# Kernel tuning notes

Measured on AMD Instinct MI355X. Metric: run time of the kernel, lower is better.

## Reference

```python
import jax, jax.numpy as jnp
import numpy as np

D_MODEL = 1024
N_HEADS = 16
D_K = D_MODEL // N_HEADS  # 64
D_FF = 2688
THETA = 10000.0
EPS = 1e-5
B, S = 2, 2048


def _rmsnorm(x, w):
    xf = x.astype(jnp.float32)
    ms = jnp.mean(xf * xf, axis=-1, keepdims=True)
    return (xf * w * jax.lax.rsqrt(ms + EPS)).astype(x.dtype)


def _rope(x, cos, sin):
    # x: [B, S, H, D_K]; cos/sin: [S, D_K//2]
    xe = x[..., 0::2]
    xo = x[..., 1::2]
    c = cos[None, :, None, :]
    s = sin[None, :, None, :]
    re = xe * c - xo * s
    ro = xe * s + xo * c
    # interleave back to even/odd layout
    return jnp.stack([re, ro], axis=-1).reshape(x.shape)


def setup_inputs() -> dict:
    key = jax.random.key(0)
    ks = jax.random.split(key, 12)
    sc = 0.02  # keep activations numerically sane (stand-in for trunc_normal init)
    return {
        "x": jax.random.normal(ks[0], (B, S, D_MODEL), dtype=jnp.float32),
        "ln1_w": jax.random.normal(ks[1], (D_MODEL,), dtype=jnp.float32) * sc + 1.0,
        "q_w": jax.random.normal(ks[2], (D_MODEL, D_MODEL), dtype=jnp.float32) * sc,
        "k_w": jax.random.normal(ks[3], (D_MODEL, D_MODEL), dtype=jnp.float32) * sc,
        "v_w": jax.random.normal(ks[4], (D_MODEL, D_MODEL), dtype=jnp.float32) * sc,
        "o_w": jax.random.normal(ks[5], (D_MODEL, D_MODEL), dtype=jnp.float32) * sc,
        "ln2_w": jax.random.normal(ks[6], (D_MODEL,), dtype=jnp.float32) * sc + 1.0,
        "w1_w": jax.random.normal(ks[7], (D_FF, D_MODEL), dtype=jnp.float32) * sc,
        "w3_w": jax.random.normal(ks[8], (D_FF, D_MODEL), dtype=jnp.float32) * sc,
        "w2_w": jax.random.normal(ks[9], (D_MODEL, D_FF), dtype=jnp.float32) * sc,
        "token_positions": jnp.arange(S, dtype=jnp.int32),
    }


def reference(x, ln1_w, q_w, k_w, v_w, o_w, ln2_w, w1_w, w3_w, w2_w, token_positions):
    b, s, _ = x.shape
    # --- pre-norm attention sublayer ---
    h = _rmsnorm(x, ln1_w)
    Q = (h @ q_w.T).reshape(b, s, N_HEADS, D_K)
    K = (h @ k_w.T).reshape(b, s, N_HEADS, D_K)
    V = (h @ v_w.T).reshape(b, s, N_HEADS, D_K)

    # RoPE tables from token positions
    pos = token_positions.astype(jnp.float32)                      # [S]
    kk = jnp.arange(D_K // 2, dtype=jnp.float32)
    inv_freq = THETA ** (-2.0 * kk / D_K)                          # [D_K/2]
    ang = pos[:, None] * inv_freq[None, :]                          # [S, D_K/2]
    cos, sin = jnp.cos(ang), jnp.sin(ang)

    Qr = _rope(Q, cos, sin)
    Kr = _rope(K, cos, sin)

    scale = 1.0 / jnp.sqrt(jnp.float32(D_K))
    scores = jnp.einsum("bqhd,bkhd->bhqk", Qr, Kr) * scale          # [B,H,S,S]
    causal = jnp.tril(jnp.ones((s, s), dtype=bool))
    scores = jnp.where(causal[None, None], scores, jnp.float32(-10000.0))
    attn = jax.nn.softmax(scores, axis=-1)
    ctx = jnp.einsum("bhqk,bkhd->bqhd", attn, V).reshape(b, s, D_MODEL)
    x1 = x + ctx @ o_w.T

    # --- pre-norm SwiGLU FFN sublayer ---
    h2 = _rmsnorm(x1, ln2_w)
    g = h2 @ w1_w.T                                                 # [B,S,D_FF]
    u = h2 @ w3_w.T
    ffn = (g * jax.nn.sigmoid(g) * u) @ w2_w.T
    return x1 + ffn
```

## Files before the change

kernel.cpp:

```cpp
#include <hip/hip_runtime.h>
#include <cstdint>

#define DM   1024
#define NH   16
#define DK   64
#define DFF  2688
#define SEQ  2048
#define BB   2
#define MTOT (BB*SEQ)

typedef __attribute__((ext_vector_type(8))) short short8;
typedef __attribute__((ext_vector_type(4))) float f32x4;

typedef const __attribute__((address_space(1))) void* gaddr_t;
typedef __attribute__((address_space(3))) void* laddr_t;
#define GLOAD_LDS16(g, l) __builtin_amdgcn_global_load_lds((gaddr_t)(g), (laddr_t)(l), 16, 0, 0)
#define MFMA16(a, b, c) __builtin_amdgcn_mfma_f32_16x16x32_bf16((a), (b), (c), 0, 0, 0)
#define WAIT_LDS() __builtin_amdgcn_s_waitcnt(0xc07f)

#define VMCNT(n) asm volatile("s_waitcnt vmcnt(" #n ")" ::: "memory")
#define BAR() do { asm volatile("" ::: "memory"); \
                   __builtin_amdgcn_s_barrier();  \
                   asm volatile("" ::: "memory"); } while (0)

__device__ __forceinline__ float bf2f(unsigned short u) {
    union { unsigned int i; float f; } v; v.i = ((unsigned int)u) << 16; return v.f;
}
__device__ __forceinline__ unsigned short f2bf(float f) {
    union { float f; unsigned int i; } v; v.f = f;
    unsigned int r = v.i + 0x7fffu + ((v.i >> 16) & 1u);
    return (unsigned short)(r >> 16);
}
__device__ __forceinline__ unsigned long long pack4bf(float a, float b, float c, float d) {
    return (unsigned long long)f2bf(a) | ((unsigned long long)f2bf(b) << 16)
         | ((unsigned long long)f2bf(c) << 32) | ((unsigned long long)f2bf(d) << 48);
}

__device__ __forceinline__ void band_swizzle(int& bx, int& by) {
    const int gx = gridDim.x;
    const int lin = blockIdx.y * gx + blockIdx.x;
    const int xcd = lin & 7, k = lin >> 3;
    by = xcd * 4 + (k & 3);
    bx = k >> 2;
}

__global__ __launch_bounds__(256)
void prep_k(const float* __restrict__ q_w, const float* __restrict__ k_w,
            const float* __restrict__ v_w, const float* __restrict__ o_w,
            const float* __restrict__ w1_w, const float* __restrict__ w3_w,
            const float* __restrict__ w2_w,
            unsigned short* __restrict__ Wqkv, unsigned short* __restrict__ Wo,
            unsigned short* __restrict__ W13, unsigned short* __restrict__ W2) {
    const int blk = blockIdx.x;
    const float* src; unsigned short* dst; int cols, rmul, roff, i;
    if (blk < 4096) {
        const int rr = blk >> 10;
        i = (blk & 1023) * 256 + threadIdx.x;
        cols = 1024; rmul = 1;
        if (rr == 0)      { src = q_w; dst = Wqkv; roff = 0; }
        else if (rr == 1) { src = k_w; dst = Wqkv; roff = 1024; }
        else if (rr == 2) { src = v_w; dst = Wqkv; roff = 2048; }
        else              { src = o_w; dst = Wo;   roff = 0; }
    } else if (blk < 6784) {
        i = (blk - 4096) * 256 + threadIdx.x; src = w1_w; dst = W13; cols = 1024; rmul = 2; roff = 0;
    } else if (blk < 9472) {
        i = (blk - 6784) * 256 + threadIdx.x; src = w3_w; dst = W13; cols = 1024; rmul = 2; roff = 1;
    } else {
        i = (blk - 9472) * 256 + threadIdx.x; src = w2_w; dst = W2;  cols = 2688; rmul = 1; roff = 0;
    }
    const int e = i * 4;
    const int r = e / cols, c = e - r * cols;
    const float4 v = *(const float4*)(src + e);
    ushort4 o;
    o.x = f2bf(v.x); o.y = f2bf(v.y); o.z = f2bf(v.z); o.w = f2bf(v.w);
    *(ushort4*)(dst + (size_t)(r * rmul + roff) * cols + c) = o;
}

__global__ __launch_bounds__(256)
void rmsnorm_k(const float* __restrict__ x, const float* __restrict__ w,
               unsigned short* __restrict__ out) {
    const int row = blockIdx.x;
    const int tid = threadIdx.x;
    const float4 v = ((const float4*)(x + (size_t)row * DM))[tid];
    float ss = v.x * v.x + v.y * v.y + v.z * v.z + v.w * v.w;
#pragma unroll
    for (int off = 32; off > 0; off >>= 1) ss += __shfl_down(ss, off, 64);
    __shared__ float sred[4];
    const int wave = tid >> 6, lane = tid & 63;
    if (lane == 0) sred[wave] = ss;
    __syncthreads();
    const float tot = sred[0] + sred[1] + sred[2] + sred[3];
    const float rinv = rsqrtf(tot * (1.0f / DM) + 1e-5f);
    const float4 wv = ((const float4*)w)[tid];
    ushort4 o;
    o.x = f2bf(v.x * wv.x * rinv);
    o.y = f2bf(v.y * wv.y * rinv);
    o.z = f2bf(v.z * wv.z * rinv);
    o.w = f2bf(v.w * wv.w * rinv);
    ((ushort4*)(out + (size_t)row * DM))[tid] = o;
}

__global__ __launch_bounds__(256)
void rope_tab_k(const int* __restrict__ pos, float* __restrict__ tab) {
    const int tid = threadIdx.x;
    const int s = blockIdx.x * 4 + (tid >> 6);
    const int t = tid & 63;
    const int kk = t & 31;
    const float ang = (float)pos[s] * __expf(-0.28782313662f * (float)kk);
    tab[s * 64 + t] = (t < 32) ? cosf(ang) : sinf(ang);
}

template <int EPI>
__global__ __launch_bounds__(512)
void gemm256(const unsigned short* __restrict__ A,
             const unsigned short* __restrict__ B,
             unsigned short* __restrict__ O0,
             unsigned short* __restrict__ O1,
             unsigned short* __restrict__ O2,
             const float* __restrict__ ROPT,
             int N, int K) {
    __shared__ unsigned short As[2][16384];
    __shared__ unsigned short Bs[2][12288];
    const int tid = threadIdx.x;
    const int wave = tid >> 6, lane = tid & 63;
    const int l15 = lane & 15, quad = lane >> 4;

    const int gx = gridDim.x;
    const int nwg = gx * gridDim.y;
    const int lin = blockIdx.y * gx + blockIdx.x;
    const int swz = (lin & 7) * (nwg >> 3) + (lin >> 3);
    const int bx = swz % gx, by = swz / gx;
    const int m0 = by * 256, n0 = bx * 192;
    const int wr = (wave >> 2) * 128, wc = (wave & 3) * 48;

    const f32x4 z4 = {0.f, 0.f, 0.f, 0.f};
    f32x4 acc[8][3];
#pragma unroll
    for (int m = 0; m < 8; m++)
#pragma unroll
        for (int n = 0; n < 3; n++) acc[m][n] = z4;

    const unsigned short* pa[4];
    int la[4];
#pragma unroll
    for (int r = 0; r < 4; r++) {
        const int s = r * 512 + tid;
        pa[r] = A + (size_t)(m0 + (s & 255)) * K + (s >> 8) * 8;
        la[r] = (r * 512 + wave * 64) * 8;
    }
    const unsigned short* pb[3];
    int lb[3];
#pragma unroll
    for (int r = 0; r < 3; r++) {
        const int s = r * 512 + tid;
        const int bk = s / 192, br = s - bk * 192;
        pb[r] = B + (size_t)(n0 + br) * K + bk * 8;
        lb[r] = (r * 512 + wave * 64) * 8;
    }

    const int nt = K >> 6;

#pragma unroll
    for (int r = 0; r < 4; r++) { GLOAD_LDS16(pa[r], &As[0][la[r]]); pa[r] += 64; }
#pragma unroll
    for (int r = 0; r < 3; r++) { GLOAD_LDS16(pb[r], &Bs[0][lb[r]]); pb[r] += 64; }

    int cur = 0;
    for (int t = 0; t < nt; ++t) {
        const int nb = cur ^ 1;
        if (t + 1 < nt) {
#pragma unroll
            for (int r = 0; r < 4; r++) { GLOAD_LDS16(pa[r], &As[nb][la[r]]); pa[r] += 64; }
            VMCNT(4);
        } else {
            VMCNT(0);
        }
        BAR();

        short8 bg[3][2];
#pragma unroll
        for (int n = 0; n < 3; n++)
#pragma unroll
            for (int kk = 0; kk < 2; kk++)
                bg[n][kk] = *(const short8*)(&Bs[cur][((quad + 4 * kk) * 192 + wc + n * 16 + l15) * 8]);

        short8 afA[2][2], afB[2][2];
#pragma unroll
        for (int m = 0; m < 2; m++)
#pragma unroll
            for (int kk = 0; kk < 2; kk++)
                afA[m][kk] = *(const short8*)(&As[cur][((quad + 4 * kk) * 256 + wr + m * 16 + l15) * 8]);

#pragma unroll
        for (int p = 0; p < 4; ++p) {
            short8 (&afC)[2][2] = (p & 1) ? afB : afA;
            short8 (&afN)[2][2] = (p & 1) ? afA : afB;
            if (p < 3) {
#pragma unroll
                for (int m = 0; m < 2; m++)
#pragma unroll
                    for (int kk = 0; kk < 2; kk++)
                        afN[m][kk] = *(const short8*)(&As[cur][((quad + 4 * kk) * 256 + wr + ((p + 1) * 2 + m) * 16 + l15) * 8]);
            }
            if (p == 1 && t + 1 < nt) {
#pragma unroll
                for (int r = 0; r < 3; r++) { GLOAD_LDS16(pb[r], &Bs[nb][lb[r]]); pb[r] += 64; }
            }
            __builtin_amdgcn_s_setprio(1);
#pragma unroll
            for (int m = 0; m < 2; m++)
#pragma unroll
                for (int n = 0; n < 3; n++)
#pragma unroll
                    for (int kk = 0; kk < 2; kk++)
                        acc[p * 2 + m][n] = MFMA16(bg[n][kk], afC[m][kk], acc[p * 2 + m][n]);
            __builtin_amdgcn_s_setprio(0);
            BAR();
        }
        cur = nb;
    }

#pragma unroll
    for (int m = 0; m < 8; m++) {
        const int r = m0 + wr + m * 16 + l15;
        if (EPI == 0) {
            const int b = r >> 11, s = r & (SEQ - 1);
            const float* rt = ROPT + s * 64;
#pragma unroll
            for (int n = 0; n < 3; n++) {
                const int cb = n0 + wc + n * 16;
                const int sec = cb >> 10;
                const int h = (cb & 1023) >> 6;
                const int cc0 = (cb & 63) + quad * 4;
                const f32x4 a = acc[m][n];
                if (sec < 2) {
                    const int p0 = cc0 >> 1;
                    const float cA = rt[p0],     sA = rt[32 + p0];
                    const float cB = rt[p0 + 1], sB = rt[32 + p0 + 1];
                    const float e0 = a[0] * cA - a[1] * sA;
                    const float o0 = a[0] * sA + a[1] * cA;
                    const float e1 = a[2] * cB - a[3] * sB;
                    const float o1 = a[2] * sB + a[3] * cB;
                    unsigned short* dst = (sec == 0) ? O0 : O1;
                    *(unsigned long long*)(dst + ((size_t)(b * NH + h) * SEQ + s) * DK + cc0) =
                        pack4bf(e0, o0, e1, o1);
                } else {
                    unsigned short* dst = O2 + ((size_t)(b * NH + h) * DK) * SEQ + s;
#pragma unroll
                    for (int tq = 0; tq < 4; tq++)
                        dst[(size_t)(cc0 + tq) * SEQ] = f2bf(a[tq]);
                }
            }
        } else {
#pragma unroll
            for (int n = 0; n < 3; n++) {
                const int cc = n0 + wc + n * 16 + quad * 4;
                const f32x4 a = acc[m][n];
                const float s1 = a[0] * a[1] / (1.f + __expf(-a[0]));
                const float s2 = a[2] * a[3] / (1.f + __expf(-a[2]));
                *(unsigned int*)(O0 + (size_t)r * (DFF) + (cc >> 1)) =
                    (unsigned int)f2bf(s1) | ((unsigned int)f2bf(s2) << 16);
            }
        }
    }
}

__global__ __launch_bounds__(256, 4)
void gemm_thin(const unsigned short* __restrict__ A,
               const unsigned short* __restrict__ B,
               float* __restrict__ Cf,
               const float* __restrict__ R,
               int N, int K) {
    __shared__ unsigned short As[8192];
    __shared__ unsigned short Bs[4096];
    const int tid = threadIdx.x;
    const int wave = tid >> 6, lane = tid & 63;
    const int l15 = lane & 15, quad = lane >> 4;
    int bx, by;
    band_swizzle(bx, by);
    const int m0 = by * 128, n0 = bx * 64;
    const int wr = (wave & 1) * 64, wc = (wave >> 1) * 32;

    const f32x4 z4 = {0.f, 0.f, 0.f, 0.f};
    f32x4 acc[4][2];
#pragma unroll
    for (int i = 0; i < 4; i++)
#pragma unroll
        for (int j = 0; j < 2; j++) acc[i][j] = z4;

    const unsigned short* ap[4];
    int al[4];
#pragma unroll
    for (int i = 0; i < 4; i++) {
        const int s = i * 256 + tid;
        ap[i] = A + (size_t)(m0 + (s & 127)) * K + (s >> 7) * 8;
        al[i] = (i * 256 + wave * 64) * 8;
    }
    const unsigned short* bp[2];
    int bl[2];
#pragma unroll
    for (int i = 0; i < 2; i++) {
        const int s = i * 256 + tid;
        bp[i] = B + (size_t)(n0 + (s & 63)) * K + (s >> 6) * 8;
        bl[i] = (i * 256 + wave * 64) * 8;
    }

    const int nk = K >> 6;
    for (int kc = 0; kc < nk; kc++) {
        __syncthreads();
#pragma unroll
        for (int i = 0; i < 4; i++) { GLOAD_LDS16(ap[i], &As[al[i]]); ap[i] += 64; }
#pragma unroll
        for (int i = 0; i < 2; i++) { GLOAD_LDS16(bp[i], &Bs[bl[i]]); bp[i] += 64; }
        __syncthreads();
#pragma unroll
        for (int h = 0; h < 2; h++) {
            short8 af[4], bg[2];
#pragma unroll
            for (int t = 0; t < 4; t++)
                af[t] = *(const short8*)(&As[((quad + 4 * h) * 128 + wr + t * 16 + l15) * 8]);
#pragma unroll
            for (int t = 0; t < 2; t++)
                bg[t] = *(const short8*)(&Bs[((quad + 4 * h) * 64 + wc + t * 16 + l15) * 8]);
#pragma unroll
            for (int i = 0; i < 4; i++)
#pragma unroll
                for (int j = 0; j < 2; j++)
                    acc[i][j] = MFMA16(bg[j], af[i], acc[i][j]);
        }
    }

#pragma unroll
    for (int i = 0; i < 4; i++) {
        const int r = m0 + wr + i * 16 + l15;
#pragma unroll
        for (int j = 0; j < 2; j++) {
            const int cc = n0 + wc + j * 16 + quad * 4;
            const size_t idx = (size_t)r * N + cc;
            const float4 rv = *(const float4*)(R + idx);
            float4 ov;
            ov.x = acc[i][j][0] + rv.x;
            ov.y = acc[i][j][1] + rv.y;
            ov.z = acc[i][j][2] + rv.z;
            ov.w = acc[i][j][3] + rv.w;
            *(float4*)(Cf + idx) = ov;
        }
    }
}

template <bool MASK>
__device__ __forceinline__ void softmax_tile(f32x4 st[4], float& li, unsigned short* Pw,
                                             int l15, int quad, int j0, int myq) {
    float lsum = 0.f;
#pragma unroll
    for (int t = 0; t < 4; t++) {
#pragma unroll
        for (int r = 0; r < 4; r++) {
            float v = st[t][r] * 0.125f;
            if (MASK) {
                const int key = j0 + t * 16 + quad * 4 + r;
                if (key > myq) v = -1e30f;
            }
            const float p = __expf(v);
            st[t][r] = p;
            lsum += p;
        }
        *(unsigned long long*)(Pw + l15 * 72 + t * 16 + quad * 4) =
            pack4bf(st[t][0], st[t][1], st[t][2], st[t][3]);
    }
    li += lsum;
}

__global__ __launch_bounds__(256, 2)
void attn_k(const unsigned short* __restrict__ Qr, const unsigned short* __restrict__ Kr,
            const unsigned short* __restrict__ Vt, unsigned short* __restrict__ ctx) {
    __shared__ unsigned short KVl[2][8192];
    __shared__ unsigned short Pl[4 * 2 * 1152];
    const int tid = threadIdx.x;
    const int wave = tid >> 6, lane = tid & 63;
    const int l15 = lane & 15, quad = lane >> 4;
    const int bh = blockIdx.y, b = bh >> 4, h = bh & 15;
    const int g = blockIdx.x;
    const int qtA = g * 4 + wave, qtB = 127 - qtA;
    const int q0A = qtA * 16, q0B = qtB * 16;
    const int countA = g + 1, countB = 32 - g;
    const unsigned short* Kb = Kr + (size_t)bh * SEQ * DK;
    const unsigned short* Vb = Vt + (size_t)bh * DK * SEQ;

    const unsigned short* QbA = Qr + ((size_t)bh * SEQ + q0A) * DK;
    const unsigned short* QbB = Qr + ((size_t)bh * SEQ + q0B) * DK;
    const short8 qfA0 = *(const short8*)(QbA + l15 * DK + quad * 8);
    const short8 qfA1 = *(const short8*)(QbA + l15 * DK + 32 + quad * 8);
    const short8 qfB0 = *(const short8*)(QbB + l15 * DK + quad * 8);
    const short8 qfB1 = *(const short8*)(QbB + l15 * DK + 32 + quad * 8);

    const int slot0 = wave * 128 + lane, slot1 = slot0 + 64;
    const int ck0 = slot0 >> 3, s0 = slot0 & 7;
    const int ck1 = slot1 >> 3, s1 = slot1 & 7;
    const unsigned short* kp0 = Kb + ck0 * 64 + (s0 ^ (ck0 & 7)) * 8;
    const unsigned short* kp1 = Kb + ck1 * 64 + (s1 ^ (ck1 & 7)) * 8;
    const unsigned short* vp0 = Vb + ck0 * 2048 + (s0 ^ (ck0 & 7)) * 8;
    const unsigned short* vp1 = Vb + ck1 * 2048 + (s1 ^ (ck1 & 7)) * 8;
    const int kb0 = wave * 1024, kb1 = kb0 + 512;

    unsigned short* PA = Pl + (wave * 2 + 0) * 1152;
    unsigned short* PB = Pl + (wave * 2 + 1) * 1152;

    const f32x4 z4 = {0.f, 0.f, 0.f, 0.f};
    f32x4 oA[4], oB[4];
#pragma unroll
    for (int d = 0; d < 4; d++) { oA[d] = z4; oB[d] = z4; }
    float liA = 0.f, liB = 0.f;
    const int myqA = q0A + l15, myqB = q0B + l15;
    const int xr = l15 & 7;

    GLOAD_LDS16(kp0, &KVl[0][kb0]);
    GLOAD_LDS16(kp1, &KVl[0][kb1]);
    GLOAD_LDS16(vp0, &KVl[0][4096 + kb0]);
    GLOAD_LDS16(vp1, &KVl[0][4096 + kb1]);
    kp0 += 4096; kp1 += 4096; vp0 += 64; vp1 += 64;

    for (int j = 0; j < countB; ++j) {
        const int bf = j & 1;
        const unsigned short* Kl = KVl[bf];
        const unsigned short* Vl = KVl[bf] + 4096;
        __syncthreads();
        if (j + 1 < countB) {
            GLOAD_LDS16(kp0, &KVl[bf ^ 1][kb0]);
            GLOAD_LDS16(kp1, &KVl[bf ^ 1][kb1]);
            GLOAD_LDS16(vp0, &KVl[bf ^ 1][4096 + kb0]);
            GLOAD_LDS16(vp1, &KVl[bf ^ 1][4096 + kb1]);
            kp0 += 4096; kp1 += 4096; vp0 += 64; vp1 += 64;
        }
        const int j0 = j * 64;
        short8 kf[4][2];
#pragma unroll
        for (int t = 0; t < 4; t++) {
            const unsigned short* kr = Kl + (t * 16 + l15) * 64;
            kf[t][0] = *(const short8*)(kr + (quad ^ xr) * 8);
            kf[t][1] = *(const short8*)(kr + ((4 + quad) ^ xr) * 8);
        }
        f32x4 stB[4];
        __builtin_amdgcn_s_setprio(1);
#pragma unroll
        for (int t = 0; t < 4; t++)
            stB[t] = MFMA16(kf[t][1], qfB1, MFMA16(kf[t][0], qfB0, z4));
        __builtin_amdgcn_s_setprio(0);
        const bool doA = (j < countA);
        if (doA) {
            f32x4 stA[4];
            __builtin_amdgcn_s_setprio(1);
#pragma unroll
            for (int t = 0; t < 4; t++)
                stA[t] = MFMA16(kf[t][1], qfA1, MFMA16(kf[t][0], qfA0, z4));
            __builtin_amdgcn_s_setprio(0);
            if (j == countA - 1) softmax_tile<true >(stA, liA, PA, l15, quad, j0, myqA);
            else                 softmax_tile<false>(stA, liA, PA, l15, quad, j0, myqA);
        }
        if (j == countB - 1) softmax_tile<true >(stB, liB, PB, l15, quad, j0, myqB);
        else                 softmax_tile<false>(stB, liB, PB, l15, quad, j0, myqB);
        WAIT_LDS();
        short8 vf[4][2];
#pragma unroll
        for (int dt = 0; dt < 4; dt++) {
            const unsigned short* vr = Vl + (dt * 16 + l15) * 64;
            vf[dt][0] = *(const short8*)(vr + (quad ^ xr) * 8);
            vf[dt][1] = *(const short8*)(vr + ((4 + quad) ^ xr) * 8);
        }
        {
            const short8 pfB0 = *(const short8*)(PB + l15 * 72 + quad * 8);
            const short8 pfB1 = *(const short8*)(PB + l15 * 72 + 32 + quad * 8);
            __builtin_amdgcn_s_setprio(1);
#pragma unroll
            for (int dt = 0; dt < 4; dt++)
                oB[dt] = MFMA16(vf[dt][1], pfB1, MFMA16(vf[dt][0], pfB0, oB[dt]));
            __builtin_amdgcn_s_setprio(0);
        }
        if (doA) {
            const short8 pfA0 = *(const short8*)(PA + l15 * 72 + quad * 8);
            const short8 pfA1 = *(const short8*)(PA + l15 * 72 + 32 + quad * 8);
            __builtin_amdgcn_s_setprio(1);
#pragma unroll
            for (int dt = 0; dt < 4; dt++)
                oA[dt] = MFMA16(vf[dt][1], pfA1, MFMA16(vf[dt][0], pfA0, oA[dt]));
            __builtin_amdgcn_s_setprio(0);
        }
    }
    liA += __shfl_xor(liA, 16, 64); liA += __shfl_xor(liA, 32, 64);
    liB += __shfl_xor(liB, 16, 64); liB += __shfl_xor(liB, 32, 64);
    const float invA = 1.0f / liA, invB = 1.0f / liB;
#pragma unroll
    for (int dt = 0; dt < 4; dt++) {
        *(unsigned long long*)(PA + l15 * 72 + dt * 16 + quad * 4) =
            pack4bf(oA[dt][0] * invA, oA[dt][1] * invA, oA[dt][2] * invA, oA[dt][3] * invA);
        *(unsigned long long*)(PB + l15 * 72 + dt * 16 + quad * 4) =
            pack4bf(oB[dt][0] * invB, oB[dt][1] * invB, oB[dt][2] * invB, oB[dt][3] * invB);
    }
    WAIT_LDS();
    const int row = lane >> 2, seg = (lane & 3) * 8;
#pragma unroll
    for (int p = 0; p < 2; p++) {
        const int cs = seg + p * 32;
        const uint4 va = *(const uint4*)(PA + row * 72 + cs);
        *(uint4*)(ctx + ((size_t)b * SEQ + q0A + row) * DM + h * DK + cs) = va;
        const uint4 vb = *(const uint4*)(PB + row * 72 + cs);
        *(uint4*)(ctx + ((size_t)b * SEQ + q0B + row) * DM + h * DK + cs) = vb;
    }
}

extern "C" void kernel_launch(void* const* d_in, const int* in_sizes, int n_in,
                              void* d_out, int out_size, void* d_ws, size_t ws_size,
                              hipStream_t stream) {
    const float* x     = (const float*)d_in[0];
    const float* ln1_w = (const float*)d_in[1];
    const float* q_w   = (const float*)d_in[2];
    const float* k_w   = (const float*)d_in[3];
    const float* v_w   = (const float*)d_in[4];
    const float* o_w   = (const float*)d_in[5];
    const float* ln2_w = (const float*)d_in[6];
    const float* w1_w  = (const float*)d_in[7];
    const float* w3_w  = (const float*)d_in[8];
    const float* w2_w  = (const float*)d_in[9];
    const int*   tpos  = (const int*)d_in[10];
    float* out = (float*)d_out;
    char* ws = (char*)d_ws;

    unsigned short* Wqkv = (unsigned short*)(ws + 0);
    unsigned short* Wo   = (unsigned short*)(ws + 6291456);
    unsigned short* W13  = (unsigned short*)(ws + 8388608);
    unsigned short* W2   = (unsigned short*)(ws + 19398656);
    float*          X1   = (float*)(ws + 24903680);
    float*          ROPT = (float*)(ws + 24903680);
    char* base = ws + 41680896;
    unsigned short* H    = (unsigned short*)(base);
    unsigned short* QR   = (unsigned short*)(base + 8388608);
    unsigned short* KR   = (unsigned short*)(base + 16777216);
    unsigned short* VT   = (unsigned short*)(base + 25165824);
    unsigned short* CTX  = (unsigned short*)(base + 33554432);
    unsigned short* H2   = (unsigned short*)(base);
    unsigned short* ACT  = (unsigned short*)(base + 41943040);

    prep_k<<<12160, 256, 0, stream>>>(q_w, k_w, v_w, o_w, w1_w, w3_w, w2_w,
                                      Wqkv, Wo, W13, W2);
    rope_tab_k<<<512, 256, 0, stream>>>(tpos, ROPT);

    rmsnorm_k<<<4096, 256, 0, stream>>>(x, ln1_w, H);
    gemm256<0><<<dim3(16, 16), 512, 0, stream>>>(H, Wqkv, QR, KR, VT, ROPT, 3072, 1024);
    attn_k<<<dim3(16, 32), 256, 0, stream>>>(QR, KR, VT, CTX);
    gemm_thin<<<dim3(16, 32), 256, 0, stream>>>(CTX, Wo, X1, x, 1024, 1024);
    rmsnorm_k<<<4096, 256, 0, stream>>>(X1, ln2_w, H2);
    gemm256<1><<<dim3(28, 16), 512, 0, stream>>>(H2, W13, ACT, nullptr, nullptr, nullptr, 5376, 1024);
    gemm_thin<<<dim3(16, 32), 256, 0, stream>>>(ACT, W2, out, X1, 1024, 2688);
}
```

Measured before the change: 408.5 us.

## Double-buffer thin GEMM with 128x128 tiles, 512 threads and XCD swizzle

Rewrites the output-projection and down-projection GEMM to use 128x128 tiles with 8 waves. LDS is now double-buffered so the next K-slice loads overlap MFMA work, with vmcnt waits and s_setprio around the MFMA bursts. Block placement changes to a chunked XCD swizzle. Launching 256 blocks instead of 512 raises per-block reuse but lowers the number of workgroups and occupancy on a 256-CU device.

```diff
diff --git a/kernel.cpp b/kernel.cpp
--- a/kernel.cpp
+++ b/kernel.cpp
@@ -34,14 +34,6 @@
 __device__ __forceinline__ unsigned long long pack4bf(float a, float b, float c, float d) {
     return (unsigned long long)f2bf(a) | ((unsigned long long)f2bf(b) << 16)
          | ((unsigned long long)f2bf(c) << 32) | ((unsigned long long)f2bf(d) << 48);
-}
-
-__device__ __forceinline__ void band_swizzle(int& bx, int& by) {
-    const int gx = gridDim.x;
-    const int lin = blockIdx.y * gx + blockIdx.x;
-    const int xcd = lin & 7, k = lin >> 3;
-    by = xcd * 4 + (k & 3);
-    bx = k >> 2;
 }
 
 __global__ __launch_bounds__(256)
@@ -265,69 +257,95 @@
     }
 }
 
-__global__ __launch_bounds__(256, 4)
+__global__ __launch_bounds__(512)
 void gemm_thin(const unsigned short* __restrict__ A,
                const unsigned short* __restrict__ B,
                float* __restrict__ Cf,
                const float* __restrict__ R,
                int N, int K) {
-    __shared__ unsigned short As[8192];
-    __shared__ unsigned short Bs[4096];
+    __shared__ unsigned short As[2][8192];
+    __shared__ unsigned short Bs[2][8192];
     const int tid = threadIdx.x;
     const int wave = tid >> 6, lane = tid & 63;
     const int l15 = lane & 15, quad = lane >> 4;
-    int bx, by;
-    band_swizzle(bx, by);
-    const int m0 = by * 128, n0 = bx * 64;
-    const int wr = (wave & 1) * 64, wc = (wave >> 1) * 32;
+
+    const int gx = gridDim.x;
+    const int nwg = gx * gridDim.y;
+    const int lin = blockIdx.y * gx + blockIdx.x;
+    const int swz = (lin & 7) * (nwg >> 3) + (lin >> 3);
+    const int bx = swz % gx, by = swz / gx;
+    const int m0 = by * 128, n0 = bx * 128;
+    const int wr = (wave >> 2) * 64, wc = (wave & 3) * 32;
 
     const f32x4 z4 = {0.f, 0.f, 0.f, 0.f};
     f32x4 acc[4][2];
 #pragma unroll
-    for (int i = 0; i < 4; i++)
-#pragma unroll
-        for (int j = 0; j < 2; j++) acc[i][j] = z4;
-
-    const unsigned short* ap[4];
-    int al[4];
-#pragma unroll
-    for (int i = 0; i < 4; i++) {
-        const int s = i * 256 + tid;
-        ap[i] = A + (size_t)(m0 + (s & 127)) * K + (s >> 7) * 8;
-        al[i] = (i * 256 + wave * 64) * 8;
-    }
-    const unsigned short* bp[2];
-    int bl[2];
-#pragma unroll
-    for (int i = 0; i < 2; i++) {
-        const int s = i * 256 + tid;
-        bp[i] = B + (size_t)(n0 + (s & 63)) * K + (s >> 6) * 8;
-        bl[i] = (i * 256 + wave * 64) * 8;
-    }
-
-    const int nk = K >> 6;
-    for (int kc = 0; kc < nk; kc++) {
-        __syncthreads();
-#pragma unroll
-        for (int i = 0; i < 4; i++) { GLOAD_LDS16(ap[i], &As[al[i]]); ap[i] += 64; }
-#pragma unroll
-        for (int i = 0; i < 2; i++) { GLOAD_LDS16(bp[i], &Bs[bl[i]]); bp[i] += 64; }
-        __syncthreads();
-#pragma unroll
-        for (int h = 0; h < 2; h++) {
-            short8 af[4], bg[2];
-#pragma unroll
-            for (int t = 0; t < 4; t++)
-                af[t] = *(const short8*)(&As[((quad + 4 * h) * 128 + wr + t * 16 + l15) * 8]);
-#pragma unroll
-            for (int t = 0; t < 2; t++)
-                bg[t] = *(const short8*)(&Bs[((quad + 4 * h) * 64 + wc + t * 16 + l15) * 8]);
-#pragma unroll
-            for (int i = 0; i < 4; i++)
-#pragma unroll
-                for (int j = 0; j < 2; j++)
-                    acc[i][j] = MFMA16(bg[j], af[i], acc[i][j]);
-        }
+    for (int m = 0; m < 4; m++)
+#pragma unroll
+        for (int n = 0; n < 2; n++) acc[m][n] = z4;
+
+    const unsigned short* pa[2];
+    const unsigned short* pb[2];
+    int la[2], lb[2];
+#pragma unroll
+    for (int r = 0; r < 2; r++) {
+        const int s = r * 512 + tid;
+        pa[r] = A + (size_t)(m0 + (s & 127)) * K + (s >> 7) * 8;
+        pb[r] = B + (size_t)(n0 + (s & 127)) * K + (s >> 7) * 8;
+        la[r] = (r * 512 + wave * 64) * 8;
+        lb[r] = la[r];
+    }
+
+    const int nt = K >> 6;
+
+#pragma unroll
+    for (int r = 0; r < 2; r++) { GLOAD_LDS16(pa[r], &As[0][la[r]]); pa[r] += 64; }
+#pragma unroll
+    for (int r = 0; r < 2; r++) { GLOAD_LDS16(pb[r], &Bs[0][lb[r]]); pb[r] += 64; }
+
+    int cur = 0;
+    for (int t = 0; t < nt; ++t) {
+        const int nb = cur ^ 1;
+        if (t + 1 < nt) {
+#pragma unroll
+            for (int r = 0; r < 2; r++) { GLOAD_LDS16(pa[r], &As[nb][la[r]]); pa[r] += 64; }
+            VMCNT(2);
+        } else {
+            VMCNT(0);
+        }
+        BAR();
+
+        short8 bg[2][2];
+#pragma unroll
+        for (int n = 0; n < 2; n++)
+#pragma unroll
+            for (int kk = 0; kk < 2; kk++)
+                bg[n][kk] = *(const short8*)(&Bs[cur][((quad + 4 * kk) * 128 + wc + n * 16 + l15) * 8]);
+
+#pragma unroll
+        for (int p = 0; p < 2; ++p) {
+            if (p == 0 && t + 1 < nt) {
+#pragma unroll
+                for (int r = 0; r < 2; r++) { GLOAD_LDS16(pb[r], &Bs[nb][lb[r]]); pb[r] += 64; }
+            }
+            short8 af[2][2];
+#pragma unroll
+            for (int m = 0; m < 2; m++)
+#pragma unroll
+                for (int kk = 0; kk < 2; kk++)
+                    af[m][kk] = *(const short8*)(&As[cur][((quad + 4 * kk) * 128 + wr + (p * 2 + m) * 16 + l15) * 8]);
+            __builtin_amdgcn_s_setprio(1);
+#pragma unroll
+            for (int m = 0; m < 2; m++)
+#pragma unroll
+                for (int n = 0; n < 2; n++)
+#pragma unroll
+                    for (int kk = 0; kk < 2; kk++)
+                        acc[p * 2 + m][n] = MFMA16(bg[n][kk], af[m][kk], acc[p * 2 + m][n]);
+            __builtin_amdgcn_s_setprio(0);
+            BAR();
+        }
+        cur = nb;
     }
 
 #pragma unroll
@@ -547,8 +565,8 @@
     rmsnorm_k<<<4096, 256, 0, stream>>>(x, ln1_w, H);
     gemm256<0><<<dim3(16, 16), 512, 0, stream>>>(H, Wqkv, QR, KR, VT, ROPT, 3072, 1024);
     attn_k<<<dim3(16, 32), 256, 0, stream>>>(QR, KR, VT, CTX);
-    gemm_thin<<<dim3(16, 32), 256, 0, stream>>>(CTX, Wo, X1, x, 1024, 1024);
+    gemm_thin<<<dim3(8, 32), 512, 0, stream>>>(CTX, Wo, X1, x, 1024, 1024);
     rmsnorm_k<<<4096, 256, 0, stream>>>(X1, ln2_w, H2);
     gemm256<1><<<dim3(28, 16), 512, 0, stream>>>(H2, W13, ACT, nullptr, nullptr, nullptr, 5376, 1024);
-    gemm_thin<<<dim3(16, 32), 256, 0, stream>>>(ACT, W2, out, X1, 1024, 2688);
-}
+    gemm_thin<<<dim3(8, 32), 512, 0, stream>>>(ACT, W2, out, X1, 1024, 2688);
+}
```

Result: faster. 395.0 us (-3.3%).
